# Performance work log

Measured on AMD Instinct MI355X. Metric: run time of the kernel, lower is better.

Reference implementation:

```python
import jax, jax.numpy as jnp
import numpy as np

N = 100000      # nodes
E = 3200000     # edges
F_IN = 512
HID = 16
C = 10


def setup_inputs() -> dict:
    key = jax.random.key(0)
    k1, k2, k3, k4 = jax.random.split(key, 4)
    x = jax.random.normal(k1, (N, F_IN), dtype=jnp.float32)
    edge_index = jax.random.randint(k2, (2, E), 0, N, dtype=jnp.int64)
    W1 = jax.random.normal(k3, (F_IN, HID), dtype=jnp.float32) * 0.05
    b1 = jnp.zeros((HID,), dtype=jnp.float32)
    W2 = jax.random.normal(k4, (HID, C), dtype=jnp.float32) * 0.05
    b2 = jnp.zeros((C,), dtype=jnp.float32)
    return {"x": x, "edge_index": edge_index, "W1": W1, "b1": b1, "W2": W2, "b2": b2}


def _gcn_norm(edge_index, n):
    # add self-loops, compute symmetric normalization deg^-1/2 * deg^-1/2
    loops = jnp.arange(n, dtype=edge_index.dtype)
    src = jnp.concatenate([edge_index[0], loops])
    dst = jnp.concatenate([edge_index[1], loops])
    deg = jax.ops.segment_sum(jnp.ones_like(dst, dtype=jnp.float32), dst, num_segments=n)
    dinv = jnp.where(deg > 0, jax.lax.rsqrt(deg), 0.0)
    norm = dinv[src] * dinv[dst]  # [E+N]
    return src, dst, norm


def _gcn_layer(h, W, b, src, dst, norm, n):
    h = h @ W                                   # project first (PyG GCNConv)
    msg = h[src] * norm[:, None]                # gather + edge scaling
    agg = jax.ops.segment_sum(msg, dst, num_segments=n)  # scatter-add
    return agg + b


def reference(x, edge_index, W1, b1, W2, b2):
    n = x.shape[0]
    src, dst, norm = _gcn_norm(edge_index, n)
    h = jax.nn.relu(_gcn_layer(x, W1, b1, src, dst, norm, n))
    # F.dropout with training=False is identity (eval mode)
    out = _gcn_layer(h, W2, b2, src, dst, norm, n)
    return jax.nn.log_softmax(out, axis=1)
```

## Files before the change

### kernel.cpp

```cpp
#include <hip/hip_runtime.h>

#define N_NODES 100000
#define N_EDGES 3200000
#define F_IN    512
#define HID     16
#define NCLS    10
#define NB      196
#define EPB     4096
#define TK      32
#define PS      12

__global__ __launch_bounds__(256) void k_binit(int* __restrict__ bcntp) {
    int i = blockIdx.x * 256 + threadIdx.x;
    if (i < NB * 16) bcntp[i] = 0;
}

__global__ __launch_bounds__(256) void k_bhist(const int* __restrict__ dst,
                                               int* __restrict__ bcntp) {
    __shared__ int h[256];
    int t = threadIdx.x;
    h[t] = 0;
    __syncthreads();
    int hi = min(N_EDGES, (int)(blockIdx.x + 1) * 8192);
    for (int e = blockIdx.x * 8192 + t; e < hi; e += 256)
        atomicAdd(&h[dst[e] >> 9], 1);
    __syncthreads();
    if (t < NB) {
        int v = h[t];
        if (v) atomicAdd(&bcntp[t * 16], v);
    }
}

__global__ __launch_bounds__(256) void k_bscan(const int* __restrict__ bcntp,
                                               int* __restrict__ boff,
                                               int* __restrict__ bcurp,
                                               int* __restrict__ row) {
    __shared__ int sh[256];
    int t = threadIdx.x;
    int v = (t < NB) ? bcntp[t * 16] : 0;
    sh[t] = v;
    __syncthreads();
    for (int off = 1; off < 256; off <<= 1) {
        int add = (t >= off) ? sh[t - off] : 0;
        __syncthreads();
        sh[t] += add;
        __syncthreads();
    }
    int excl = sh[t] - v;
    if (t < NB) { boff[t] = excl; bcurp[t * 16] = excl; }
    if (t == 0) { boff[NB] = N_EDGES; row[N_NODES] = N_EDGES; }
}

__global__ __launch_bounds__(256) void k_bpart(const int* __restrict__ ei,
                                               int* __restrict__ bcurp,
                                               int* __restrict__ part) {
    __shared__ int cnt_sh[256], base_sh[256];
    int t = threadIdx.x;
    cnt_sh[t] = 0;
    __syncthreads();
    int base = blockIdx.x * EPB;
    int pk[16], bk[16], rk[16];
#pragma unroll
    for (int j = 0; j < 16; ++j) {
        int e = base + j * 256 + t;
        if (e < N_EDGES) {
            int s = ei[e], d = ei[N_EDGES + e];
            bk[j] = d >> 9;
            pk[j] = ((d & 511) << 17) | s;
            rk[j] = atomicAdd(&cnt_sh[bk[j]], 1);
        } else bk[j] = -1;
    }
    __syncthreads();
    if (t < NB && cnt_sh[t] > 0)
        base_sh[t] = atomicAdd(&bcurp[t * 16], cnt_sh[t]);
    __syncthreads();
#pragma unroll
    for (int j = 0; j < 16; ++j)
        if (bk[j] >= 0) part[base_sh[bk[j]] + rk[j]] = pk[j];
}

__global__ __launch_bounds__(256) void k_bucket(const int* __restrict__ boff,
                                                const int* __restrict__ part,
                                                int* __restrict__ row,
                                                float* __restrict__ dinv,
                                                int* __restrict__ srcs) {
    __shared__ int cnt[512], ofs[512], sc[256];
    int t = threadIdx.x;
    int b = blockIdx.x;
    int e0 = boff[b], e1 = boff[b + 1];
    int nbase = b << 9;
    cnt[t] = 0; cnt[t + 256] = 0;
    __syncthreads();
    for (int e = e0 + t; e < e1; e += 256)
        atomicAdd(&cnt[part[e] >> 17], 1);
    __syncthreads();
    int a0 = cnt[2 * t], a1 = cnt[2 * t + 1];
    sc[t] = a0 + a1;
    __syncthreads();
    for (int off = 1; off < 256; off <<= 1) {
        int add = (t >= off) ? sc[t - off] : 0;
        __syncthreads();
        sc[t] += add;
        __syncthreads();
    }
    int excl = sc[t] - (a0 + a1);
    ofs[2 * t] = excl;
    ofs[2 * t + 1] = excl + a0;
    __syncthreads();
#pragma unroll
    for (int r = 0; r < 2; ++r) {
        int ln = t + r * 256;
        int n = nbase + ln;
        if (n < N_NODES) {
            row[n] = e0 + ofs[ln];
            dinv[n] = rsqrtf((float)(cnt[ln] + 1));
        }
    }
    __syncthreads();
    for (int e = e0 + t; e < e1; e += 256) {
        int pp = part[e];
        int pos = atomicAdd(&ofs[pp >> 17], 1);
        srcs[e0 + pos] = pp & 0x1FFFF;
    }
}

__global__ __launch_bounds__(128) void k_gemm1(const float* __restrict__ x,
                                               const float* __restrict__ W1,
                                               const float* __restrict__ dinv,
                                               float* __restrict__ h1s) {
    __shared__ float xs[128][TK + 1];
    __shared__ float wchunk[TK * 16];
    const int t = threadIdx.x;
    const int nbase = blockIdx.x * 128;
    const int f4 = t & 7;
    const int r0 = t >> 3;

    float4 pre[8];
#pragma unroll
    for (int p = 0; p < 8; ++p) {
        int n = nbase + r0 + p * 16;
        pre[p] = (n < N_NODES) ? ((const float4*)(x + (size_t)n * F_IN))[f4]
                               : make_float4(0.f, 0.f, 0.f, 0.f);
    }
    float4 wpre = ((const float4*)W1)[t];

    float acc[16];
#pragma unroll
    for (int j = 0; j < 16; ++j) acc[j] = 0.f;

    for (int c = 0; c < F_IN; c += TK) {
#pragma unroll
        for (int p = 0; p < 8; ++p) {
            int r = r0 + p * 16;
            xs[r][f4 * 4 + 0] = pre[p].x;
            xs[r][f4 * 4 + 1] = pre[p].y;
            xs[r][f4 * 4 + 2] = pre[p].z;
            xs[r][f4 * 4 + 3] = pre[p].w;
        }
        ((float4*)wchunk)[t] = wpre;
        __syncthreads();
        if (c + TK < F_IN) {
#pragma unroll
            for (int p = 0; p < 8; ++p) {
                int n = nbase + r0 + p * 16;
                pre[p] = (n < N_NODES)
                           ? ((const float4*)(x + (size_t)n * F_IN + c + TK))[f4]
                           : make_float4(0.f, 0.f, 0.f, 0.f);
            }
            wpre = ((const float4*)(W1 + (c + TK) * 16))[t];
        }
#pragma unroll
        for (int k = 0; k < TK; ++k) {
            float xv = xs[t][k];
            const float4* wk = (const float4*)&wchunk[k * 16];
            float4 wa = wk[0], wb = wk[1], wc = wk[2], wd = wk[3];
            acc[0]  = fmaf(xv, wa.x, acc[0]);
            acc[1]  = fmaf(xv, wa.y, acc[1]);
            acc[2]  = fmaf(xv, wa.z, acc[2]);
            acc[3]  = fmaf(xv, wa.w, acc[3]);
            acc[4]  = fmaf(xv, wb.x, acc[4]);
            acc[5]  = fmaf(xv, wb.y, acc[5]);
            acc[6]  = fmaf(xv, wb.z, acc[6]);
            acc[7]  = fmaf(xv, wb.w, acc[7]);
            acc[8]  = fmaf(xv, wc.x, acc[8]);
            acc[9]  = fmaf(xv, wc.y, acc[9]);
            acc[10] = fmaf(xv, wc.z, acc[10]);
            acc[11] = fmaf(xv, wc.w, acc[11]);
            acc[12] = fmaf(xv, wd.x, acc[12]);
            acc[13] = fmaf(xv, wd.y, acc[13]);
            acc[14] = fmaf(xv, wd.z, acc[14]);
            acc[15] = fmaf(xv, wd.w, acc[15]);
        }
        __syncthreads();
    }

    int n = nbase + t;
    if (n < N_NODES) {
        float dn = dinv[n];
        float4* o = (float4*)(h1s + (size_t)n * HID);
        o[0] = make_float4(acc[0] * dn,  acc[1] * dn,  acc[2] * dn,  acc[3] * dn);
        o[1] = make_float4(acc[4] * dn,  acc[5] * dn,  acc[6] * dn,  acc[7] * dn);
        o[2] = make_float4(acc[8] * dn,  acc[9] * dn,  acc[10] * dn, acc[11] * dn);
        o[3] = make_float4(acc[12] * dn, acc[13] * dn, acc[14] * dn, acc[15] * dn);
    }
}

__global__ __launch_bounds__(256) void k_edge1g(const int* __restrict__ row,
                                                const int* __restrict__ srcs,
                                                const float* __restrict__ dinv,
                                                const float* __restrict__ h1s,
                                                const float* __restrict__ b1,
                                                float* __restrict__ agg1) {
    int t = blockIdx.x * 256 + threadIdx.x;
    if (t >= N_NODES * 4) return;
    int n = t >> 2, q = t & 3;
    const float4* h4 = (const float4*)h1s;
    float4 sum = h4[n * 4 + q];
    int k = row[n], k1 = row[n + 1];
    for (; k + 4 <= k1; k += 4) {
        int s0 = srcs[k], s1 = srcs[k + 1], s2 = srcs[k + 2], s3 = srcs[k + 3];
        float4 v0 = h4[s0 * 4 + q], v1 = h4[s1 * 4 + q];
        float4 v2 = h4[s2 * 4 + q], v3 = h4[s3 * 4 + q];
        sum.x += (v0.x + v1.x) + (v2.x + v3.x);
        sum.y += (v0.y + v1.y) + (v2.y + v3.y);
        sum.z += (v0.z + v1.z) + (v2.z + v3.z);
        sum.w += (v0.w + v1.w) + (v2.w + v3.w);
    }
    for (; k < k1; ++k) {
        float4 v = h4[srcs[k] * 4 + q];
        sum.x += v.x; sum.y += v.y; sum.z += v.z; sum.w += v.w;
    }
    float dn = dinv[n];
    float4 bb = ((const float4*)b1)[q];
    float4 r;
    r.x = fmaxf(fmaf(dn, sum.x, bb.x), 0.f);
    r.y = fmaxf(fmaf(dn, sum.y, bb.y), 0.f);
    r.z = fmaxf(fmaf(dn, sum.z, bb.z), 0.f);
    r.w = fmaxf(fmaf(dn, sum.w, bb.w), 0.f);
    ((float4*)agg1)[n * 4 + q] = r;
}

__global__ __launch_bounds__(256) void k_gemm2(const float* __restrict__ agg1,
                                               const float* __restrict__ W2,
                                               const float* __restrict__ dinv,
                                               float* __restrict__ ps) {
    int t = blockIdx.x * 256 + threadIdx.x;
    if (t >= N_NODES * 3) return;
    int n = t / 3, c4 = t - n * 3;
    int c0 = c4 * 4;
    const float4* a4 = (const float4*)(agg1 + n * HID);
    float4 a0 = a4[0], a1 = a4[1], a2 = a4[2], a3 = a4[3];
    float aj[16] = {a0.x, a0.y, a0.z, a0.w, a1.x, a1.y, a1.z, a1.w,
                    a2.x, a2.y, a2.z, a2.w, a3.x, a3.y, a3.z, a3.w};
    float4 acc = make_float4(0.f, 0.f, 0.f, 0.f);
#pragma unroll
    for (int j = 0; j < HID; ++j) {
        float av = aj[j];
        acc.x = fmaf(av, W2[j * NCLS + c0], acc.x);
        acc.y = fmaf(av, W2[j * NCLS + c0 + 1], acc.y);
        acc.z = fmaf(av, (c0 + 2 < NCLS) ? W2[j * NCLS + c0 + 2] : 0.f, acc.z);
        acc.w = fmaf(av, (c0 + 3 < NCLS) ? W2[j * NCLS + c0 + 3] : 0.f, acc.w);
    }
    float dn = dinv[n];
    ((float4*)ps)[n * 3 + c4] =
        make_float4(acc.x * dn, acc.y * dn, acc.z * dn, acc.w * dn);
}

__global__ __launch_bounds__(256) void k_edge2g(const int* __restrict__ row,
                                                const int* __restrict__ srcs,
                                                const float* __restrict__ dinv,
                                                const float* __restrict__ ps,
                                                const float* __restrict__ b2,
                                                float* __restrict__ out) {
    int t = blockIdx.x * 256 + threadIdx.x;
    if (t >= N_NODES * 4) return;
    int n = t >> 2, q = t & 3;
    int qc = (q < 3) ? q : 2;
    const float4* p4 = (const float4*)ps;
    float4 sum = p4[n * 3 + qc];
    int k = row[n], k1 = row[n + 1];
    for (; k + 4 <= k1; k += 4) {
        int s0 = srcs[k], s1 = srcs[k + 1], s2 = srcs[k + 2], s3 = srcs[k + 3];
        float4 v0 = p4[s0 * 3 + qc], v1 = p4[s1 * 3 + qc];
        float4 v2 = p4[s2 * 3 + qc], v3 = p4[s3 * 3 + qc];
        sum.x += (v0.x + v1.x) + (v2.x + v3.x);
        sum.y += (v0.y + v1.y) + (v2.y + v3.y);
        sum.z += (v0.z + v1.z) + (v2.z + v3.z);
        sum.w += (v0.w + v1.w) + (v2.w + v3.w);
    }
    for (; k < k1; ++k) {
        float4 v = p4[srcs[k] * 3 + qc];
        sum.x += v.x; sum.y += v.y; sum.z += v.z; sum.w += v.w;
    }
    float dn = dinv[n];
    int c0 = qc * 4;
    float4 val;
    val.x = fmaf(dn, sum.x, b2[c0]);
    val.y = fmaf(dn, sum.y, b2[c0 + 1]);
    val.z = (c0 + 2 < NCLS) ? fmaf(dn, sum.z, b2[c0 + 2]) : -1e30f;
    val.w = (c0 + 3 < NCLS) ? fmaf(dn, sum.w, b2[c0 + 3]) : -1e30f;
    float m = fmaxf(fmaxf(val.x, val.y), fmaxf(val.z, val.w));
    m = fmaxf(m, __shfl_xor(m, 1));
    m = fmaxf(m, __shfl_xor(m, 2));
    float se = __expf(val.x - m) + __expf(val.y - m)
             + __expf(val.z - m) + __expf(val.w - m);
    if (q == 3) se = 0.f;
    se += __shfl_xor(se, 1);
    se += __shfl_xor(se, 2);
    float l = m + __logf(se);
    if (q < 2) {
        float* o = out + n * NCLS + c0;
        o[0] = val.x - l; o[1] = val.y - l; o[2] = val.z - l; o[3] = val.w - l;
    } else if (q == 2) {
        float* o = out + n * NCLS + 8;
        o[0] = val.x - l; o[1] = val.y - l;
    }
}

extern "C" void kernel_launch(void* const* d_in, const int* in_sizes, int n_in,
                              void* d_out, int out_size, void* d_ws, size_t ws_size,
                              hipStream_t stream) {
    const float* x  = (const float*)d_in[0];
    const int*   ei = (const int*)d_in[1];
    const float* W1 = (const float*)d_in[2];
    const float* b1 = (const float*)d_in[3];
    const float* W2 = (const float*)d_in[4];
    const float* b2 = (const float*)d_in[5];
    float* out = (float*)d_out;

    int* w = (int*)d_ws;
    float* dinv = (float*)w;
    int*   row   = w + 102400;
    int*   bcntp = w + 204816;
    int*   bcurp = w + 207952;
    int*   boff  = w + 211088;
    int*   part  = w + 211344;
    int*   srcs  = w + 3411344;
    float* h1s   = (float*)(w + 6611344);
    float* agg1  = (float*)(w + 8249744);
    float* ps    = (float*)(w + 9888144);

    k_binit<<<(NB * 16 + 255) / 256, 256, 0, stream>>>(bcntp);
    k_bhist<<<(N_EDGES + 8191) / 8192, 256, 0, stream>>>(ei + N_EDGES, bcntp);
    k_bscan<<<1, 256, 0, stream>>>(bcntp, boff, bcurp, row);
    k_bpart<<<(N_EDGES + EPB - 1) / EPB, 256, 0, stream>>>(ei, bcurp, part);
    k_bucket<<<NB, 256, 0, stream>>>(boff, part, row, dinv, srcs);

    k_gemm1 <<<(N_NODES + 127) / 128, 128, 0, stream>>>(x, W1, dinv, h1s);
    k_edge1g<<<(N_NODES * 4 + 255) / 256, 256, 0, stream>>>(row, srcs, dinv, h1s, b1, agg1);
    k_gemm2 <<<(N_NODES * 3 + 255) / 256, 256, 0, stream>>>(agg1, W2, dinv, ps);
    k_edge2g<<<(N_NODES * 4 + 255) / 256, 256, 0, stream>>>(row, srcs, dinv, ps, b2, out);
}
```

Baseline: 511.2 us.

## Store gathered node features in fp16, fuse second GEMM into first aggregation

Intermediate node features (h1 and the layer-2 projection) are stored as packed half2 instead of fp32, halving the bytes moved by the random gathers in both aggregation kernels. The layer-2 projection by W2 is fused into the layer-1 aggregation kernel through a cross-lane shuffle reduction, which removes one launch and the agg1 round trip through memory. The gather loops are unrolled to eight edges with a predicated tail, and the bucket kernel's atomic loops are unrolled by four. The cost is reduced precision in the intermediate features, which could affect accuracy tolerance.

```diff
diff --git a/kernel.cpp b/kernel.cpp
--- a/kernel.cpp
+++ b/kernel.cpp
@@ -1,4 +1,5 @@
 #include <hip/hip_runtime.h>
+#include <hip/hip_fp16.h>
 
 #define N_NODES 100000
 #define N_EDGES 3200000
@@ -8,7 +9,17 @@
 #define NB      196
 #define EPB     4096
 #define TK      32
-#define PS      12
+
+union H2F { __half2 h; float f; };
+__device__ __forceinline__ float h2f_pack(float a, float b) {
+    H2F u; u.h = __floats2half2_rn(a, b); return u.f;
+}
+__device__ __forceinline__ void h2f_add(float raw, float& a, float& b) {
+    H2F u; u.f = raw; float2 v = __half22float2(u.h); a += v.x; b += v.y;
+}
+__device__ __forceinline__ void acc4(float2 raw, float& a, float& b, float& c, float& d) {
+    h2f_add(raw.x, a, b); h2f_add(raw.y, c, d);
+}
 
 __global__ __launch_bounds__(256) void k_binit(int* __restrict__ bcntp) {
     int i = blockIdx.x * 256 + threadIdx.x;
@@ -91,8 +102,16 @@
     int nbase = b << 9;
     cnt[t] = 0; cnt[t + 256] = 0;
     __syncthreads();
-    for (int e = e0 + t; e < e1; e += 256)
-        atomicAdd(&cnt[part[e] >> 17], 1);
+    for (int e = e0 + t; e < e1; e += 1024) {
+        int p0 = part[e];
+        int p1 = (e + 256 < e1) ? part[e + 256] : -1;
+        int p2 = (e + 512 < e1) ? part[e + 512] : -1;
+        int p3 = (e + 768 < e1) ? part[e + 768] : -1;
+        atomicAdd(&cnt[p0 >> 17], 1);
+        if (p1 >= 0) atomicAdd(&cnt[p1 >> 17], 1);
+        if (p2 >= 0) atomicAdd(&cnt[p2 >> 17], 1);
+        if (p3 >= 0) atomicAdd(&cnt[p3 >> 17], 1);
+    }
     __syncthreads();
     int a0 = cnt[2 * t], a1 = cnt[2 * t + 1];
     sc[t] = a0 + a1;
@@ -117,17 +136,23 @@
         }
     }
     __syncthreads();
-    for (int e = e0 + t; e < e1; e += 256) {
-        int pp = part[e];
-        int pos = atomicAdd(&ofs[pp >> 17], 1);
-        srcs[e0 + pos] = pp & 0x1FFFF;
+    for (int e = e0 + t; e < e1; e += 1024) {
+        int p0 = part[e];
+        int p1 = (e + 256 < e1) ? part[e + 256] : -1;
+        int p2 = (e + 512 < e1) ? part[e + 512] : -1;
+        int p3 = (e + 768 < e1) ? part[e + 768] : -1;
+        int o0 = atomicAdd(&ofs[p0 >> 17], 1);
+        srcs[e0 + o0] = p0 & 0x1FFFF;
+        if (p1 >= 0) { int o = atomicAdd(&ofs[p1 >> 17], 1); srcs[e0 + o] = p1 & 0x1FFFF; }
+        if (p2 >= 0) { int o = atomicAdd(&ofs[p2 >> 17], 1); srcs[e0 + o] = p2 & 0x1FFFF; }
+        if (p3 >= 0) { int o = atomicAdd(&ofs[p3 >> 17], 1); srcs[e0 + o] = p3 & 0x1FFFF; }
     }
 }
 
 __global__ __launch_bounds__(128) void k_gemm1(const float* __restrict__ x,
                                                const float* __restrict__ W1,
                                                const float* __restrict__ dinv,
-                                               float* __restrict__ h1s) {
+                                               __half* __restrict__ h1h) {
     __shared__ float xs[128][TK + 1];
     __shared__ float wchunk[TK * 16];
     const int t = threadIdx.x;
@@ -197,123 +222,139 @@
     int n = nbase + t;
     if (n < N_NODES) {
         float dn = dinv[n];
-        float4* o = (float4*)(h1s + (size_t)n * HID);
-        o[0] = make_float4(acc[0] * dn,  acc[1] * dn,  acc[2] * dn,  acc[3] * dn);
-        o[1] = make_float4(acc[4] * dn,  acc[5] * dn,  acc[6] * dn,  acc[7] * dn);
-        o[2] = make_float4(acc[8] * dn,  acc[9] * dn,  acc[10] * dn, acc[11] * dn);
-        o[3] = make_float4(acc[12] * dn, acc[13] * dn, acc[14] * dn, acc[15] * dn);
-    }
-}
-
-__global__ __launch_bounds__(256) void k_edge1g(const int* __restrict__ row,
+        float4 o0 = make_float4(h2f_pack(acc[0]  * dn, acc[1]  * dn),
+                                h2f_pack(acc[2]  * dn, acc[3]  * dn),
+                                h2f_pack(acc[4]  * dn, acc[5]  * dn),
+                                h2f_pack(acc[6]  * dn, acc[7]  * dn));
+        float4 o1 = make_float4(h2f_pack(acc[8]  * dn, acc[9]  * dn),
+                                h2f_pack(acc[10] * dn, acc[11] * dn),
+                                h2f_pack(acc[12] * dn, acc[13] * dn),
+                                h2f_pack(acc[14] * dn, acc[15] * dn));
+        float4* o = (float4*)(h1h + (size_t)n * 16);
+        o[0] = o0; o[1] = o1;
+    }
+}
+
+__global__ __launch_bounds__(256) void k_edge1f(const int* __restrict__ row,
                                                 const int* __restrict__ srcs,
                                                 const float* __restrict__ dinv,
-                                                const float* __restrict__ h1s,
+                                                const __half* __restrict__ h1h,
                                                 const float* __restrict__ b1,
-                                                float* __restrict__ agg1) {
+                                                const float* __restrict__ W2,
+                                                __half* __restrict__ ps) {
+    __shared__ float w2s[HID * NCLS];
+    if (threadIdx.x < HID * NCLS) w2s[threadIdx.x] = W2[threadIdx.x];
+    __syncthreads();
     int t = blockIdx.x * 256 + threadIdx.x;
     if (t >= N_NODES * 4) return;
     int n = t >> 2, q = t & 3;
-    const float4* h4 = (const float4*)h1s;
-    float4 sum = h4[n * 4 + q];
+    const float2* h2 = (const float2*)h1h;
+    float s0 = 0.f, s1 = 0.f, s2 = 0.f, s3 = 0.f;
+    acc4(h2[n * 4 + q], s0, s1, s2, s3);
     int k = row[n], k1 = row[n + 1];
-    for (; k + 4 <= k1; k += 4) {
-        int s0 = srcs[k], s1 = srcs[k + 1], s2 = srcs[k + 2], s3 = srcs[k + 3];
-        float4 v0 = h4[s0 * 4 + q], v1 = h4[s1 * 4 + q];
-        float4 v2 = h4[s2 * 4 + q], v3 = h4[s3 * 4 + q];
-        sum.x += (v0.x + v1.x) + (v2.x + v3.x);
-        sum.y += (v0.y + v1.y) + (v2.y + v3.y);
-        sum.z += (v0.z + v1.z) + (v2.z + v3.z);
-        sum.w += (v0.w + v1.w) + (v2.w + v3.w);
-    }
-    for (; k < k1; ++k) {
-        float4 v = h4[srcs[k] * 4 + q];
-        sum.x += v.x; sum.y += v.y; sum.z += v.z; sum.w += v.w;
+    for (; k + 8 <= k1; k += 8) {
+        int a0 = srcs[k],     a1 = srcs[k + 1], a2 = srcs[k + 2], a3 = srcs[k + 3];
+        int a4 = srcs[k + 4], a5 = srcs[k + 5], a6 = srcs[k + 6], a7 = srcs[k + 7];
+        float2 v0 = h2[a0 * 4 + q], v1 = h2[a1 * 4 + q];
+        float2 v2 = h2[a2 * 4 + q], v3 = h2[a3 * 4 + q];
+        float2 v4 = h2[a4 * 4 + q], v5 = h2[a5 * 4 + q];
+        float2 v6 = h2[a6 * 4 + q], v7 = h2[a7 * 4 + q];
+        acc4(v0, s0, s1, s2, s3); acc4(v1, s0, s1, s2, s3);
+        acc4(v2, s0, s1, s2, s3); acc4(v3, s0, s1, s2, s3);
+        acc4(v4, s0, s1, s2, s3); acc4(v5, s0, s1, s2, s3);
+        acc4(v6, s0, s1, s2, s3); acc4(v7, s0, s1, s2, s3);
+    }
+    if (k < k1) {
+        int sb = srcs[k];
+        int idx[8]; float2 vv[8];
+#pragma unroll
+        for (int j = 0; j < 8; ++j) idx[j] = (k + j < k1) ? srcs[k + j] : sb;
+#pragma unroll
+        for (int j = 0; j < 8; ++j) vv[j] = h2[idx[j] * 4 + q];
+#pragma unroll
+        for (int j = 0; j < 8; ++j)
+            if (k + j < k1) acc4(vv[j], s0, s1, s2, s3);
     }
     float dn = dinv[n];
-    float4 bb = ((const float4*)b1)[q];
-    float4 r;
-    r.x = fmaxf(fmaf(dn, sum.x, bb.x), 0.f);
-    r.y = fmaxf(fmaf(dn, sum.y, bb.y), 0.f);
-    r.z = fmaxf(fmaf(dn, sum.z, bb.z), 0.f);
-    r.w = fmaxf(fmaf(dn, sum.w, bb.w), 0.f);
-    ((float4*)agg1)[n * 4 + q] = r;
-}
-
-__global__ __launch_bounds__(256) void k_gemm2(const float* __restrict__ agg1,
-                                               const float* __restrict__ W2,
-                                               const float* __restrict__ dinv,
-                                               float* __restrict__ ps) {
-    int t = blockIdx.x * 256 + threadIdx.x;
-    if (t >= N_NODES * 3) return;
-    int n = t / 3, c4 = t - n * 3;
-    int c0 = c4 * 4;
-    const float4* a4 = (const float4*)(agg1 + n * HID);
-    float4 a0 = a4[0], a1 = a4[1], a2 = a4[2], a3 = a4[3];
-    float aj[16] = {a0.x, a0.y, a0.z, a0.w, a1.x, a1.y, a1.z, a1.w,
-                    a2.x, a2.y, a2.z, a2.w, a3.x, a3.y, a3.z, a3.w};
-    float4 acc = make_float4(0.f, 0.f, 0.f, 0.f);
-#pragma unroll
-    for (int j = 0; j < HID; ++j) {
-        float av = aj[j];
-        acc.x = fmaf(av, W2[j * NCLS + c0], acc.x);
-        acc.y = fmaf(av, W2[j * NCLS + c0 + 1], acc.y);
-        acc.z = fmaf(av, (c0 + 2 < NCLS) ? W2[j * NCLS + c0 + 2] : 0.f, acc.z);
-        acc.w = fmaf(av, (c0 + 3 < NCLS) ? W2[j * NCLS + c0 + 3] : 0.f, acc.w);
-    }
-    float dn = dinv[n];
-    ((float4*)ps)[n * 3 + c4] =
-        make_float4(acc.x * dn, acc.y * dn, acc.z * dn, acc.w * dn);
-}
-
-__global__ __launch_bounds__(256) void k_edge2g(const int* __restrict__ row,
+    int c0 = q * 4;
+    float r0 = fmaxf(fmaf(dn, s0, b1[c0 + 0]), 0.f);
+    float r1 = fmaxf(fmaf(dn, s1, b1[c0 + 1]), 0.f);
+    float r2 = fmaxf(fmaf(dn, s2, b1[c0 + 2]), 0.f);
+    float r3 = fmaxf(fmaf(dn, s3, b1[c0 + 3]), 0.f);
+    float p[NCLS];
+#pragma unroll
+    for (int c = 0; c < NCLS; ++c)
+        p[c] = r0 * w2s[(c0 + 0) * NCLS + c] + r1 * w2s[(c0 + 1) * NCLS + c]
+             + r2 * w2s[(c0 + 2) * NCLS + c] + r3 * w2s[(c0 + 3) * NCLS + c];
+#pragma unroll
+    for (int c = 0; c < NCLS; ++c) {
+        p[c] += __shfl_xor(p[c], 1);
+        p[c] += __shfl_xor(p[c], 2);
+    }
+    float o0, o1, o2, o3;
+    if (q == 0)      { o0 = p[0]; o1 = p[1]; o2 = p[2]; o3 = p[3]; }
+    else if (q == 1) { o0 = p[4]; o1 = p[5]; o2 = p[6]; o3 = p[7]; }
+    else if (q == 2) { o0 = p[8]; o1 = p[9]; o2 = 0.f;  o3 = 0.f;  }
+    else             { o0 = 0.f;  o1 = 0.f;  o2 = 0.f;  o3 = 0.f;  }
+    float2 st = make_float2(h2f_pack(o0 * dn, o1 * dn), h2f_pack(o2 * dn, o3 * dn));
+    ((float2*)ps)[n * 4 + q] = st;
+}
+
+__global__ __launch_bounds__(256) void k_edge2f(const int* __restrict__ row,
                                                 const int* __restrict__ srcs,
                                                 const float* __restrict__ dinv,
-                                                const float* __restrict__ ps,
+                                                const __half* __restrict__ ps,
                                                 const float* __restrict__ b2,
                                                 float* __restrict__ out) {
     int t = blockIdx.x * 256 + threadIdx.x;
     if (t >= N_NODES * 4) return;
     int n = t >> 2, q = t & 3;
-    int qc = (q < 3) ? q : 2;
-    const float4* p4 = (const float4*)ps;
-    float4 sum = p4[n * 3 + qc];
+    const float2* p2 = (const float2*)ps;
+    float s0 = 0.f, s1 = 0.f, s2 = 0.f, s3 = 0.f;
+    acc4(p2[n * 4 + q], s0, s1, s2, s3);
     int k = row[n], k1 = row[n + 1];
-    for (; k + 4 <= k1; k += 4) {
-        int s0 = srcs[k], s1 = srcs[k + 1], s2 = srcs[k + 2], s3 = srcs[k + 3];
-        float4 v0 = p4[s0 * 3 + qc], v1 = p4[s1 * 3 + qc];
-        float4 v2 = p4[s2 * 3 + qc], v3 = p4[s3 * 3 + qc];
-        sum.x += (v0.x + v1.x) + (v2.x + v3.x);
-        sum.y += (v0.y + v1.y) + (v2.y + v3.y);
-        sum.z += (v0.z + v1.z) + (v2.z + v3.z);
-        sum.w += (v0.w + v1.w) + (v2.w + v3.w);
-    }
-    for (; k < k1; ++k) {
-        float4 v = p4[srcs[k] * 3 + qc];
-        sum.x += v.x; sum.y += v.y; sum.z += v.z; sum.w += v.w;
+    for (; k + 8 <= k1; k += 8) {
+        int a0 = srcs[k],     a1 = srcs[k + 1], a2 = srcs[k + 2], a3 = srcs[k + 3];
+        int a4 = srcs[k + 4], a5 = srcs[k + 5], a6 = srcs[k + 6], a7 = srcs[k + 7];
+        float2 v0 = p2[a0 * 4 + q], v1 = p2[a1 * 4 + q];
+        float2 v2 = p2[a2 * 4 + q], v3 = p2[a3 * 4 + q];
+        float2 v4 = p2[a4 * 4 + q], v5 = p2[a5 * 4 + q];
+        float2 v6 = p2[a6 * 4 + q], v7 = p2[a7 * 4 + q];
+        acc4(v0, s0, s1, s2, s3); acc4(v1, s0, s1, s2, s3);
+        acc4(v2, s0, s1, s2, s3); acc4(v3, s0, s1, s2, s3);
+        acc4(v4, s0, s1, s2, s3); acc4(v5, s0, s1, s2, s3);
+        acc4(v6, s0, s1, s2, s3); acc4(v7, s0, s1, s2, s3);
+    }
+    if (k < k1) {
+        int sb = srcs[k];
+        int idx[8]; float2 vv[8];
+#pragma unroll
+        for (int j = 0; j < 8; ++j) idx[j] = (k + j < k1) ? srcs[k + j] : sb;
+#pragma unroll
+        for (int j = 0; j < 8; ++j) vv[j] = p2[idx[j] * 4 + q];
+#pragma unroll
+        for (int j = 0; j < 8; ++j)
+            if (k + j < k1) acc4(vv[j], s0, s1, s2, s3);
     }
     float dn = dinv[n];
-    int c0 = qc * 4;
-    float4 val;
-    val.x = fmaf(dn, sum.x, b2[c0]);
-    val.y = fmaf(dn, sum.y, b2[c0 + 1]);
-    val.z = (c0 + 2 < NCLS) ? fmaf(dn, sum.z, b2[c0 + 2]) : -1e30f;
-    val.w = (c0 + 3 < NCLS) ? fmaf(dn, sum.w, b2[c0 + 3]) : -1e30f;
-    float m = fmaxf(fmaxf(val.x, val.y), fmaxf(val.z, val.w));
+    int c0 = q * 4;
+    float v0 = (c0 + 0 < NCLS) ? fmaf(dn, s0, b2[c0 + 0]) : -1e30f;
+    float v1 = (c0 + 1 < NCLS) ? fmaf(dn, s1, b2[c0 + 1]) : -1e30f;
+    float v2 = (c0 + 2 < NCLS) ? fmaf(dn, s2, b2[c0 + 2]) : -1e30f;
+    float v3 = (c0 + 3 < NCLS) ? fmaf(dn, s3, b2[c0 + 3]) : -1e30f;
+    float m = fmaxf(fmaxf(v0, v1), fmaxf(v2, v3));
     m = fmaxf(m, __shfl_xor(m, 1));
     m = fmaxf(m, __shfl_xor(m, 2));
-    float se = __expf(val.x - m) + __expf(val.y - m)
-             + __expf(val.z - m) + __expf(val.w - m);
-    if (q == 3) se = 0.f;
+    float se = __expf(v0 - m) + __expf(v1 - m) + __expf(v2 - m) + __expf(v3 - m);
     se += __shfl_xor(se, 1);
     se += __shfl_xor(se, 2);
     float l = m + __logf(se);
     if (q < 2) {
         float* o = out + n * NCLS + c0;
-        o[0] = val.x - l; o[1] = val.y - l; o[2] = val.z - l; o[3] = val.w - l;
+        o[0] = v0 - l; o[1] = v1 - l; o[2] = v2 - l; o[3] = v3 - l;
     } else if (q == 2) {
         float* o = out + n * NCLS + 8;
-        o[0] = val.x - l; o[1] = val.y - l;
+        o[0] = v0 - l; o[1] = v1 - l;
     }
 }
 
@@ -329,16 +370,15 @@
     float* out = (float*)d_out;
 
     int* w = (int*)d_ws;
-    float* dinv = (float*)w;
-    int*   row   = w + 102400;
-    int*   bcntp = w + 204816;
-    int*   bcurp = w + 207952;
-    int*   boff  = w + 211088;
-    int*   part  = w + 211344;
-    int*   srcs  = w + 3411344;
-    float* h1s   = (float*)(w + 6611344);
-    float* agg1  = (float*)(w + 8249744);
-    float* ps    = (float*)(w + 9888144);
+    float*  dinv  = (float*)w;
+    int*    row   = w + 102400;
+    int*    bcntp = w + 204816;
+    int*    bcurp = w + 207952;
+    int*    boff  = w + 211088;
+    int*    part  = w + 211344;
+    int*    srcs  = w + 3411344;
+    __half* h1h   = (__half*)(w + 6611344);
+    __half* ps    = (__half*)(w + 9888144);
 
     k_binit<<<(NB * 16 + 255) / 256, 256, 0, stream>>>(bcntp);
     k_bhist<<<(N_EDGES + 8191) / 8192, 256, 0, stream>>>(ei + N_EDGES, bcntp);
@@ -346,8 +386,7 @@
     k_bpart<<<(N_EDGES + EPB - 1) / EPB, 256, 0, stream>>>(ei, bcurp, part);
     k_bucket<<<NB, 256, 0, stream>>>(boff, part, row, dinv, srcs);
 
-    k_gemm1 <<<(N_NODES + 127) / 128, 128, 0, stream>>>(x, W1, dinv, h1s);
-    k_edge1g<<<(N_NODES * 4 + 255) / 256, 256, 0, stream>>>(row, srcs, dinv, h1s, b1, agg1);
-    k_gemm2 <<<(N_NODES * 3 + 255) / 256, 256, 0, stream>>>(agg1, W2, dinv, ps);
-    k_edge2g<<<(N_NODES * 4 + 255) / 256, 256, 0, stream>>>(row, srcs, dinv, ps, b2, out);
-}
+    k_gemm1 <<<(N_NODES + 127) / 128, 128, 0, stream>>>(x, W1, dinv, h1h);
+    k_edge1f<<<(N_NODES * 4 + 255) / 256, 256, 0, stream>>>(row, srcs, dinv, h1h, b1, W2, ps);
+    k_edge2f<<<(N_NODES * 4 + 255) / 256, 256, 0, stream>>>(row, srcs, dinv, ps, b2, out);
+}
```

After: 454.4 us. 1.13x faster.
